# Performance work log

Measured on AMD Instinct MI355X. Metric: run time of the kernel, lower is better.

Reference implementation:

```python
import jax, jax.numpy as jnp
import numpy as np
from jax import lax

K, N = 256, 65536

def setup_inputs() -> dict:
    key = jax.random.key(0)
    k1, k2, k3 = jax.random.split(key, 3)
    # obs: non-negative event counts [K, N]
    obs = jax.random.uniform(k1, (K, N), dtype=jnp.float32) * 4.0
    # Beta ~ U(1, 3) [K]
    Beta = 1.0 + 2.0 * jax.random.uniform(k2, (K,), dtype=jnp.float32)
    # Alpha ~ U(0, 0.01) [K, K]
    Alpha = 0.01 * jax.random.uniform(k3, (K, K), dtype=jnp.float32)
    return {"obs": obs, "Beta": Beta, "Alpha": Alpha}

def reference(obs, Beta, Alpha):
    # obs: [K, N], Beta: [K], Alpha: [K, K]
    Kk, Nn = obs.shape
    Mu0 = obs.mean(axis=1) / 10.0 + 0.01            # [K] background rate
    decay = jnp.exp(-Beta)                          # [K]

    # Exponential kernel sum S[t] = sum_{tp<t} obs[:,tp] * Beta * exp(-(t-tp)*Beta)
    # admits recursion H[t] = exp(-Beta) * (H[t-1] + obs[:, t-1]), S[t] = Beta * H[t]
    def step(h, o_prev):
        h_new = decay * (h + o_prev)
        return h_new, h_new

    _, H = lax.scan(step, jnp.zeros((Kk,), obs.dtype), obs[:, :Nn - 1].T)  # [N-1, K]
    S = H * Beta                                    # [N-1, K]
    # lam1[:, t] = softplus(Alpha @ S[t]) for t >= 1; lam1[:, 0] = 0 (by original code)
    lam = jax.nn.softplus(jnp.einsum('jk,tk->tj', Alpha, S))  # [N-1, K]
    lams1 = jnp.concatenate([jnp.zeros((Kk, 1), obs.dtype), lam.T], axis=1)  # [K, N]
    lams0 = jnp.broadcast_to(Mu0[:, None], (Kk, Nn))          # [K, N]

    Nloglams = obs * jnp.log(lams0 + lams1 + 1e-5)
    loglik = (Nloglams - lams0 - lams1).sum()
    return loglik, lams0, lams1
```

## Files before the change

### kernel.cpp

```cpp
#include <hip/hip_runtime.h>
#include <math.h>

#define KK 256
#define NN 65536
#define TT 128
#define WW 16
#define TPAD 264

typedef __bf16 bf16x8 __attribute__((ext_vector_type(8)));
typedef float f32x4 __attribute__((ext_vector_type(4)));

__global__ __launch_bounds__(512) void prep_kernel(const float* __restrict__ obs,
                                                   const float* __restrict__ Alpha,
                                                   float* __restrict__ mu0,
                                                   __bf16* __restrict__ AlphaB,
                                                   float* __restrict__ out) {
  const int j = blockIdx.x;
  const int tid = threadIdx.x;
  if (tid < KK) AlphaB[(size_t)j * KK + tid] = (__bf16)Alpha[(size_t)j * KK + tid];
  const float4* p = (const float4*)(obs + (size_t)j * NN) + tid;
  float s = 0.f;
#pragma unroll
  for (int i = 0; i < 32; ++i) {
    float4 v = p[i * 512];
    s += (v.x + v.y) + (v.z + v.w);
  }
  __shared__ float red[512];
  red[tid] = s;
  __syncthreads();
  for (int off = 256; off > 0; off >>= 1) {
    if (tid < off) red[tid] += red[tid + off];
    __syncthreads();
  }
  const float m = red[0] * (1.0f / NN) * 0.1f + 0.01f;
  if (tid == 0) mu0[j] = m;

  float* row0 = out + 1 + (size_t)j * NN;
  if (tid < 3) row0[tid] = m;
  if (tid == 3) row0[NN - 1] = m;
  float4* p4 = (float4*)(row0 + 3);
  const float4 mv = {m, m, m, m};
  for (int i = tid; i < (NN - 4) / 4; i += 512) p4[i] = mv;
}

__global__ __launch_bounds__(512, 4) void main_kernel(const float* __restrict__ obs,
                                                      const float* __restrict__ Beta,
                                                      const float* __restrict__ mu0,
                                                      const __bf16* __restrict__ AlphaB,
                                                      float* __restrict__ out,
                                                      float* __restrict__ bpart) {
  __shared__ __bf16 Slds[TT][TPAD];
  const int tid = threadIdx.x;
  const int bid = blockIdx.x;
  const int tb = ((bid & 7) << 6) | (bid >> 3);
  const int t0 = tb * TT;

  {
    const int k = tid & 255;
    const int c = tid >> 8;
    const int tbase = t0 + 64 * c;
    const float beta = Beta[k];
    const float decay = expf(-beta);
    const float* row = obs + (size_t)k * NN;
    float g = 0.f;
    if (tbase > 0) {
      const float4* p = (const float4*)(row + tbase - WW);
#pragma unroll
      for (int i = 0; i < WW / 4; ++i) {
        float4 v = p[i];
        g = decay * (g + v.x);
        g = decay * (g + v.y);
        g = decay * (g + v.z);
        g = decay * (g + v.w);
      }
    }
    const int r0 = 64 * c;
    Slds[r0][k] = (__bf16)(beta * g);
    const float4* q = (const float4*)(row + tbase);
#pragma unroll
    for (int i = 0; i < 15; ++i) {
      float4 v = q[i];
      g = decay * (g + v.x); Slds[r0 + 4 * i + 1][k] = (__bf16)(beta * g);
      g = decay * (g + v.y); Slds[r0 + 4 * i + 2][k] = (__bf16)(beta * g);
      g = decay * (g + v.z); Slds[r0 + 4 * i + 3][k] = (__bf16)(beta * g);
      g = decay * (g + v.w); Slds[r0 + 4 * i + 4][k] = (__bf16)(beta * g);
    }
    {
      float4 v = q[15];
      g = decay * (g + v.x); Slds[r0 + 61][k] = (__bf16)(beta * g);
      g = decay * (g + v.y); Slds[r0 + 62][k] = (__bf16)(beta * g);
      g = decay * (g + v.z); Slds[r0 + 63][k] = (__bf16)(beta * g);
    }
  }
  __syncthreads();

  const int wave = tid >> 6;
  const int wj = wave & 3, wc = wave >> 2;
  const int lane = tid & 63;
  const int lquad = lane >> 4;
  const int l16 = lane & 15;

  f32x4 acc[4][4];
#pragma unroll
  for (int a = 0; a < 4; ++a)
#pragma unroll
    for (int b = 0; b < 4; ++b) acc[a][b] = (f32x4){0.f, 0.f, 0.f, 0.f};

  const __bf16* Abase = AlphaB + (size_t)(wj * 64 + l16) * KK + lquad * 8;
  for (int k0 = 0; k0 < KK; k0 += 32) {
    bf16x8 afrag[4], bfrag[4];
#pragma unroll
    for (int js = 0; js < 4; ++js)
      afrag[js] = *(const bf16x8*)(Abase + (size_t)js * 16 * KK + k0);
#pragma unroll
    for (int ts = 0; ts < 4; ++ts)
      bfrag[ts] = *(const bf16x8*)&Slds[wc * 64 + ts * 16 + l16][k0 + lquad * 8];
#pragma unroll
    for (int js = 0; js < 4; ++js)
#pragma unroll
      for (int ts = 0; ts < 4; ++ts)
        acc[js][ts] = __builtin_amdgcn_mfma_f32_16x16x32_bf16(
            afrag[js], bfrag[ts], acc[js][ts], 0, 0, 0);
  }

  float partial = 0.f;
  float* lams1 = out + 1 + (size_t)KK * NN;
  const int tcol = t0 + wc * 64;
#pragma unroll
  for (int js = 0; js < 4; ++js) {
#pragma unroll
    for (int r = 0; r < 4; ++r) {
      const int j = wj * 64 + js * 16 + lquad * 4 + r;
      const float m = mu0[j];
      const size_t rowoff = (size_t)j * NN + tcol + l16;
#pragma unroll
      for (int ts = 0; ts < 4; ++ts) {
        float v = acc[js][ts][r];
        float lam = v + __logf(1.f + __expf(-v));
        if (tcol + ts * 16 + l16 == 0) lam = 0.f;
        lams1[rowoff + ts * 16] = lam;
        const float o = obs[rowoff + ts * 16];
        partial += o * __logf(m + lam + 1e-5f) - m - lam;
      }
    }
  }

#pragma unroll
  for (int off = 32; off > 0; off >>= 1)
    partial += __shfl_down(partial, off, 64);
  __syncthreads();
  float* red = (float*)&Slds[0][0];
  if (lane == 0) red[wave] = partial;
  __syncthreads();
  if (tid == 0) {
    float s = 0.f;
#pragma unroll
    for (int w = 0; w < 8; ++w) s += red[w];
    bpart[bid] = s;
  }
}

__global__ __launch_bounds__(256) void finish_kernel(const float* __restrict__ bpart,
                                                     float* __restrict__ out) {
  const int tid = threadIdx.x;
  float s = bpart[tid] + bpart[tid + 256];
#pragma unroll
  for (int off = 32; off > 0; off >>= 1)
    s += __shfl_down(s, off, 64);
  __shared__ float red[4];
  if ((tid & 63) == 0) red[tid >> 6] = s;
  __syncthreads();
  if (tid == 0) out[0] = (red[0] + red[1]) + (red[2] + red[3]);
}

extern "C" void kernel_launch(void* const* d_in, const int* in_sizes, int n_in,
                              void* d_out, int out_size, void* d_ws, size_t ws_size,
                              hipStream_t stream) {
  const float* obs   = (const float*)d_in[0];
  const float* Beta  = (const float*)d_in[1];
  const float* Alpha = (const float*)d_in[2];
  float* out = (float*)d_out;

  float* mu0 = (float*)d_ws;
  __bf16* AlphaB = (__bf16*)(mu0 + 256);
  float* bpart = (float*)(AlphaB + (size_t)KK * KK);

  hipLaunchKernelGGL(prep_kernel, dim3(KK), dim3(512), 0, stream, obs, Alpha,
                     mu0, AlphaB, out);
  hipLaunchKernelGGL(main_kernel, dim3(NN / TT), dim3(512), 0, stream,
                     obs, Beta, mu0, AlphaB, out, bpart);
  hipLaunchKernelGGL(finish_kernel, dim3(1), dim3(256), 0, stream, bpart, out);
}
```

Before: 231.1 us.

## Double time tile per block and use nontemporal stores for outputs

Doubles the time tile from 128 to 256 columns per block, giving each wave an 8-wide accumulator set so every Alpha fragment loaded from global memory feeds twice as many MFMAs. This halves the block count and the warm-up recurrence overhead, and the finish kernel now reduces 256 partials. Output stores to lams0 and lams1 switch to nontemporal stores to reduce cache pollution. In exchange, occupancy drops (launch bound lowered to 2 blocks per CU, LDS doubled to about 135 KB per block) and register pressure rises.

```diff
diff --git a/kernel.cpp b/kernel.cpp
--- a/kernel.cpp
+++ b/kernel.cpp
@@ -3,7 +3,7 @@
 
 #define KK 256
 #define NN 65536
-#define TT 128
+#define TT 256
 #define WW 16
 #define TPAD 264
 
@@ -38,12 +38,12 @@
   float* row0 = out + 1 + (size_t)j * NN;
   if (tid < 3) row0[tid] = m;
   if (tid == 3) row0[NN - 1] = m;
-  float4* p4 = (float4*)(row0 + 3);
-  const float4 mv = {m, m, m, m};
-  for (int i = tid; i < (NN - 4) / 4; i += 512) p4[i] = mv;
+  f32x4* p4 = (f32x4*)(row0 + 3);
+  const f32x4 mv = {m, m, m, m};
+  for (int i = tid; i < (NN - 4) / 4; i += 512) __builtin_nontemporal_store(mv, p4 + i);
 }
 
-__global__ __launch_bounds__(512, 4) void main_kernel(const float* __restrict__ obs,
+__global__ __launch_bounds__(512, 2) void main_kernel(const float* __restrict__ obs,
                                                       const float* __restrict__ Beta,
                                                       const float* __restrict__ mu0,
                                                       const __bf16* __restrict__ AlphaB,
@@ -52,13 +52,13 @@
   __shared__ __bf16 Slds[TT][TPAD];
   const int tid = threadIdx.x;
   const int bid = blockIdx.x;
-  const int tb = ((bid & 7) << 6) | (bid >> 3);
+  const int tb = ((bid & 7) << 5) | (bid >> 3);
   const int t0 = tb * TT;
 
   {
     const int k = tid & 255;
     const int c = tid >> 8;
-    const int tbase = t0 + 64 * c;
+    const int tbase = t0 + (c << 7);
     const float beta = Beta[k];
     const float decay = expf(-beta);
     const float* row = obs + (size_t)k * NN;
@@ -74,11 +74,11 @@
         g = decay * (g + v.w);
       }
     }
-    const int r0 = 64 * c;
+    const int r0 = c << 7;
     Slds[r0][k] = (__bf16)(beta * g);
     const float4* q = (const float4*)(row + tbase);
 #pragma unroll
-    for (int i = 0; i < 15; ++i) {
+    for (int i = 0; i < 31; ++i) {
       float4 v = q[i];
       g = decay * (g + v.x); Slds[r0 + 4 * i + 1][k] = (__bf16)(beta * g);
       g = decay * (g + v.y); Slds[r0 + 4 * i + 2][k] = (__bf16)(beta * g);
@@ -86,10 +86,10 @@
       g = decay * (g + v.w); Slds[r0 + 4 * i + 4][k] = (__bf16)(beta * g);
     }
     {
-      float4 v = q[15];
-      g = decay * (g + v.x); Slds[r0 + 61][k] = (__bf16)(beta * g);
-      g = decay * (g + v.y); Slds[r0 + 62][k] = (__bf16)(beta * g);
-      g = decay * (g + v.z); Slds[r0 + 63][k] = (__bf16)(beta * g);
+      float4 v = q[31];
+      g = decay * (g + v.x); Slds[r0 + 125][k] = (__bf16)(beta * g);
+      g = decay * (g + v.y); Slds[r0 + 126][k] = (__bf16)(beta * g);
+      g = decay * (g + v.z); Slds[r0 + 127][k] = (__bf16)(beta * g);
     }
   }
   __syncthreads();
@@ -100,32 +100,37 @@
   const int lquad = lane >> 4;
   const int l16 = lane & 15;
 
-  f32x4 acc[4][4];
+  f32x4 acc[4][8];
 #pragma unroll
   for (int a = 0; a < 4; ++a)
 #pragma unroll
-    for (int b = 0; b < 4; ++b) acc[a][b] = (f32x4){0.f, 0.f, 0.f, 0.f};
+    for (int b = 0; b < 8; ++b) acc[a][b] = (f32x4){0.f, 0.f, 0.f, 0.f};
 
   const __bf16* Abase = AlphaB + (size_t)(wj * 64 + l16) * KK + lquad * 8;
   for (int k0 = 0; k0 < KK; k0 += 32) {
-    bf16x8 afrag[4], bfrag[4];
+    bf16x8 afrag[4];
 #pragma unroll
     for (int js = 0; js < 4; ++js)
       afrag[js] = *(const bf16x8*)(Abase + (size_t)js * 16 * KK + k0);
 #pragma unroll
-    for (int ts = 0; ts < 4; ++ts)
-      bfrag[ts] = *(const bf16x8*)&Slds[wc * 64 + ts * 16 + l16][k0 + lquad * 8];
+    for (int th = 0; th < 2; ++th) {
+      bf16x8 bfrag[4];
 #pragma unroll
-    for (int js = 0; js < 4; ++js)
+      for (int q4 = 0; q4 < 4; ++q4)
+        bfrag[q4] = *(const bf16x8*)&Slds[wc * 128 + (th * 4 + q4) * 16 + l16]
+                                        [k0 + lquad * 8];
 #pragma unroll
-      for (int ts = 0; ts < 4; ++ts)
-        acc[js][ts] = __builtin_amdgcn_mfma_f32_16x16x32_bf16(
-            afrag[js], bfrag[ts], acc[js][ts], 0, 0, 0);
+      for (int js = 0; js < 4; ++js)
+#pragma unroll
+        for (int q4 = 0; q4 < 4; ++q4)
+          acc[js][th * 4 + q4] = __builtin_amdgcn_mfma_f32_16x16x32_bf16(
+              afrag[js], bfrag[q4], acc[js][th * 4 + q4], 0, 0, 0);
+    }
   }
 
   float partial = 0.f;
   float* lams1 = out + 1 + (size_t)KK * NN;
-  const int tcol = t0 + wc * 64;
+  const int tcol = t0 + wc * 128;
 #pragma unroll
   for (int js = 0; js < 4; ++js) {
 #pragma unroll
@@ -134,11 +139,11 @@
       const float m = mu0[j];
       const size_t rowoff = (size_t)j * NN + tcol + l16;
 #pragma unroll
-      for (int ts = 0; ts < 4; ++ts) {
+      for (int ts = 0; ts < 8; ++ts) {
         float v = acc[js][ts][r];
         float lam = v + __logf(1.f + __expf(-v));
         if (tcol + ts * 16 + l16 == 0) lam = 0.f;
-        lams1[rowoff + ts * 16] = lam;
+        __builtin_nontemporal_store(lam, &lams1[rowoff + ts * 16]);
         const float o = obs[rowoff + ts * 16];
         partial += o * __logf(m + lam + 1e-5f) - m - lam;
       }
@@ -163,7 +168,7 @@
 __global__ __launch_bounds__(256) void finish_kernel(const float* __restrict__ bpart,
                                                      float* __restrict__ out) {
   const int tid = threadIdx.x;
-  float s = bpart[tid] + bpart[tid + 256];
+  float s = bpart[tid];
 #pragma unroll
   for (int off = 32; off > 0; off >>= 1)
     s += __shfl_down(s, off, 64);
```

New measurement: 246.4 us. 6.6% more time.

## Fuse row-mean into main kernel and move loglik into separate per-row pass

Applied to the files above, without the earlier changes.

The background-rate row sums are now computed as per-chunk partial sums inside the main kernel's recursion loop, removing the standalone obs pass in the prep kernel. Writing lams0 and the log-likelihood reduction move to a new per-row kernel that reads back lams1 and obs, and accumulates into the output with atomics. This removes one full read of obs before the main kernel, but adds a full read of lams1 plus another obs pass after it. The final sum now uses atomic adds, so its summation order is nondeterministic.

```diff
diff --git a/kernel.cpp b/kernel.cpp
--- a/kernel.cpp
+++ b/kernel.cpp
@@ -6,49 +6,25 @@
 #define TT 128
 #define WW 16
 #define TPAD 264
+#define NB (NN / TT)
+#define NCHUNK (NB * 2)
 
 typedef __bf16 bf16x8 __attribute__((ext_vector_type(8)));
 typedef float f32x4 __attribute__((ext_vector_type(4)));
 
-__global__ __launch_bounds__(512) void prep_kernel(const float* __restrict__ obs,
-                                                   const float* __restrict__ Alpha,
-                                                   float* __restrict__ mu0,
-                                                   __bf16* __restrict__ AlphaB,
-                                                   float* __restrict__ out) {
-  const int j = blockIdx.x;
-  const int tid = threadIdx.x;
-  if (tid < KK) AlphaB[(size_t)j * KK + tid] = (__bf16)Alpha[(size_t)j * KK + tid];
-  const float4* p = (const float4*)(obs + (size_t)j * NN) + tid;
-  float s = 0.f;
-#pragma unroll
-  for (int i = 0; i < 32; ++i) {
-    float4 v = p[i * 512];
-    s += (v.x + v.y) + (v.z + v.w);
-  }
-  __shared__ float red[512];
-  red[tid] = s;
-  __syncthreads();
-  for (int off = 256; off > 0; off >>= 1) {
-    if (tid < off) red[tid] += red[tid + off];
-    __syncthreads();
-  }
-  const float m = red[0] * (1.0f / NN) * 0.1f + 0.01f;
-  if (tid == 0) mu0[j] = m;
-
-  float* row0 = out + 1 + (size_t)j * NN;
-  if (tid < 3) row0[tid] = m;
-  if (tid == 3) row0[NN - 1] = m;
-  float4* p4 = (float4*)(row0 + 3);
-  const float4 mv = {m, m, m, m};
-  for (int i = tid; i < (NN - 4) / 4; i += 512) p4[i] = mv;
+__global__ __launch_bounds__(256) void alpha_kernel(const float* __restrict__ Alpha,
+                                                    __bf16* __restrict__ AlphaB,
+                                                    float* __restrict__ out) {
+  const int i = blockIdx.x * 256 + threadIdx.x;
+  AlphaB[i] = (__bf16)Alpha[i];
+  if (i == 0) out[0] = 0.f;
 }
 
 __global__ __launch_bounds__(512, 4) void main_kernel(const float* __restrict__ obs,
                                                       const float* __restrict__ Beta,
-                                                      const float* __restrict__ mu0,
                                                       const __bf16* __restrict__ AlphaB,
                                                       float* __restrict__ out,
-                                                      float* __restrict__ bpart) {
+                                                      float* __restrict__ P) {
   __shared__ __bf16 Slds[TT][TPAD];
   const int tid = threadIdx.x;
   const int bid = blockIdx.x;
@@ -58,7 +34,7 @@
   {
     const int k = tid & 255;
     const int c = tid >> 8;
-    const int tbase = t0 + 64 * c;
+    const int tbase = t0 + (c << 6);
     const float beta = Beta[k];
     const float decay = expf(-beta);
     const float* row = obs + (size_t)k * NN;
@@ -74,12 +50,14 @@
         g = decay * (g + v.w);
       }
     }
-    const int r0 = 64 * c;
+    const int r0 = c << 6;
     Slds[r0][k] = (__bf16)(beta * g);
     const float4* q = (const float4*)(row + tbase);
+    float s = 0.f;
 #pragma unroll
     for (int i = 0; i < 15; ++i) {
       float4 v = q[i];
+      s += (v.x + v.y) + (v.z + v.w);
       g = decay * (g + v.x); Slds[r0 + 4 * i + 1][k] = (__bf16)(beta * g);
       g = decay * (g + v.y); Slds[r0 + 4 * i + 2][k] = (__bf16)(beta * g);
       g = decay * (g + v.z); Slds[r0 + 4 * i + 3][k] = (__bf16)(beta * g);
@@ -87,10 +65,12 @@
     }
     {
       float4 v = q[15];
+      s += (v.x + v.y) + (v.z + v.w);
       g = decay * (g + v.x); Slds[r0 + 61][k] = (__bf16)(beta * g);
       g = decay * (g + v.y); Slds[r0 + 62][k] = (__bf16)(beta * g);
       g = decay * (g + v.z); Slds[r0 + 63][k] = (__bf16)(beta * g);
     }
+    P[(size_t)(2 * bid + c) * KK + k] = s;
   }
   __syncthreads();
 
@@ -123,7 +103,6 @@
             afrag[js], bfrag[ts], acc[js][ts], 0, 0, 0);
   }
 
-  float partial = 0.f;
   float* lams1 = out + 1 + (size_t)KK * NN;
   const int tcol = t0 + wc * 64;
 #pragma unroll
@@ -131,7 +110,6 @@
 #pragma unroll
     for (int r = 0; r < 4; ++r) {
       const int j = wj * 64 + js * 16 + lquad * 4 + r;
-      const float m = mu0[j];
       const size_t rowoff = (size_t)j * NN + tcol + l16;
 #pragma unroll
       for (int ts = 0; ts < 4; ++ts) {
@@ -139,38 +117,55 @@
         float lam = v + __logf(1.f + __expf(-v));
         if (tcol + ts * 16 + l16 == 0) lam = 0.f;
         lams1[rowoff + ts * 16] = lam;
-        const float o = obs[rowoff + ts * 16];
-        partial += o * __logf(m + lam + 1e-5f) - m - lam;
       }
     }
+  }
+}
+
+__global__ __launch_bounds__(512) void loglik_kernel(const float* __restrict__ obs,
+                                                     const float* __restrict__ P,
+                                                     float* __restrict__ out) {
+  const int j = blockIdx.x;
+  const int tid = threadIdx.x;
+
+  float s = 0.f;
+#pragma unroll
+  for (int c = 0; c < NCHUNK / 512; ++c)
+    s += P[(size_t)(tid + c * 512) * KK + j];
+  __shared__ float red[512];
+  red[tid] = s;
+  __syncthreads();
+  for (int off = 256; off > 0; off >>= 1) {
+    if (tid < off) red[tid] += red[tid + off];
+    __syncthreads();
+  }
+  const float m = red[0] * (1.0f / NN) * 0.1f + 0.01f;
+
+  const float* orow = obs + (size_t)j * NN;
+  float* l0row = out + 1 + (size_t)j * NN;
+  float* l1row = l0row + (size_t)KK * NN;
+  float partial = 0.f;
+#pragma unroll 8
+  for (int i = 0; i < NN / 512; ++i) {
+    const int t = tid + i * 512;
+    const float l1 = l1row[t];
+    const float o = orow[t];
+    l0row[t] = m;
+    partial += o * __logf(m + l1 + 1e-5f) - m - l1;
   }
 
 #pragma unroll
   for (int off = 32; off > 0; off >>= 1)
     partial += __shfl_down(partial, off, 64);
   __syncthreads();
-  float* red = (float*)&Slds[0][0];
-  if (lane == 0) red[wave] = partial;
+  if ((tid & 63) == 0) red[tid >> 6] = partial;
   __syncthreads();
   if (tid == 0) {
-    float s = 0.f;
+    float t = 0.f;
 #pragma unroll
-    for (int w = 0; w < 8; ++w) s += red[w];
-    bpart[bid] = s;
+    for (int w = 0; w < 8; ++w) t += red[w];
+    atomicAdd(out, t);
   }
-}
-
-__global__ __launch_bounds__(256) void finish_kernel(const float* __restrict__ bpart,
-                                                     float* __restrict__ out) {
-  const int tid = threadIdx.x;
-  float s = bpart[tid] + bpart[tid + 256];
-#pragma unroll
-  for (int off = 32; off > 0; off >>= 1)
-    s += __shfl_down(s, off, 64);
-  __shared__ float red[4];
-  if ((tid & 63) == 0) red[tid >> 6] = s;
-  __syncthreads();
-  if (tid == 0) out[0] = (red[0] + red[1]) + (red[2] + red[3]);
 }
 
 extern "C" void kernel_launch(void* const* d_in, const int* in_sizes, int n_in,
@@ -181,13 +176,11 @@
   const float* Alpha = (const float*)d_in[2];
   float* out = (float*)d_out;
 
-  float* mu0 = (float*)d_ws;
-  __bf16* AlphaB = (__bf16*)(mu0 + 256);
-  float* bpart = (float*)(AlphaB + (size_t)KK * KK);
+  __bf16* AlphaB = (__bf16*)d_ws;
+  float* P = (float*)(AlphaB + (size_t)KK * KK);
 
-  hipLaunchKernelGGL(prep_kernel, dim3(KK), dim3(512), 0, stream, obs, Alpha,
-                     mu0, AlphaB, out);
-  hipLaunchKernelGGL(main_kernel, dim3(NN / TT), dim3(512), 0, stream,
-                     obs, Beta, mu0, AlphaB, out, bpart);
-  hipLaunchKernelGGL(finish_kernel, dim3(1), dim3(256), 0, stream, bpart, out);
+  hipLaunchKernelGGL(alpha_kernel, dim3(KK), dim3(256), 0, stream, Alpha, AlphaB, out);
+  hipLaunchKernelGGL(main_kernel, dim3(NB), dim3(512), 0, stream,
+                     obs, Beta, AlphaB, out, P);
+  hipLaunchKernelGGL(loglik_kernel, dim3(KK), dim3(512), 0, stream, obs, P, out);
 }
```

Result: no change. 232.8 us (+0.7%).
